# Kernel tuning notes

Measured on AMD Instinct MI355X. Metric: run time of the kernel, lower is better.

## Reference

```python
import jax, jax.numpy as jnp
import numpy as np

B, N, M, C = 2, 16384, 16, 64
D_HIDDEN = 64  # int(d * hidden_scale) with d=64, hidden_scale=1
BN_EPS = 1e-5


def setup_inputs() -> dict:
    key = jax.random.key(0)
    ks = jax.random.split(key, 10)
    s = 1.0 / np.sqrt(C)
    return {
        "center_feat": jax.random.normal(ks[0], (B, N, C), jnp.float32),
        "neighbor_feat": jax.random.normal(ks[1], (B, N, M, C), jnp.float32),
        "pos_enc": jax.random.normal(ks[2], (B, N, M, C), jnp.float32),
        "Wq": jax.random.normal(ks[3], (C, C), jnp.float32) * s,      # nn.Linear(d, d), no bias
        "Wkv": jax.random.normal(ks[4], (2 * C, C), jnp.float32) * s, # nn.Linear(d, 2d), no bias
        "W1": jax.random.normal(ks[5], (D_HIDDEN, C), jnp.float32) * s,  # 1x1 Conv2d(d, d_hidden)
        "bn_gamma": jnp.ones((D_HIDDEN,), jnp.float32),
        "bn_beta": jnp.zeros((D_HIDDEN,), jnp.float32),
        "bn_mean": jax.random.normal(ks[6], (D_HIDDEN,), jnp.float32) * 0.1,
        "bn_var": jax.random.uniform(ks[7], (D_HIDDEN,), jnp.float32, 0.5, 1.5),
        "W2": jax.random.normal(ks[8], (C, D_HIDDEN), jnp.float32) * (1.0 / np.sqrt(D_HIDDEN)),  # 1x1 Conv2d(d_hidden, d)
    }


def reference(center_feat, neighbor_feat, pos_enc, Wq, Wkv, W1, bn_gamma, bn_beta, bn_mean, bn_var, W2):
    # Q = Linear(center_feat): (B, N, C)
    Q = jnp.einsum("bnc,dc->bnd", center_feat, Wq)
    # K, V = chunk(Linear(neighbor_feat), 2): each (B, N, M, C)
    KV = jnp.einsum("bnmc,dc->bnmd", neighbor_feat, Wkv)
    K, V = jnp.split(KV, 2, axis=-1)
    # broadcast subtract + pos enc: (B, N, M, C)
    attn = Q[:, :, None, :] - K + pos_enc
    # mlp: 1x1 conv -> BN (eval, running stats) -> ReLU -> 1x1 conv (channel = last axis)
    h = jnp.einsum("bnmc,hc->bnmh", attn, W1)
    h = (h - bn_mean) * (bn_gamma / jnp.sqrt(bn_var + BN_EPS)) + bn_beta
    h = jax.nn.relu(h)
    attn = jnp.einsum("bnmh,ch->bnmc", h, W2)
    # softmax over neighbor dim M, weighted sum
    w = jax.nn.softmax(attn, axis=2)
    return jnp.sum(w * (V + pos_enc), axis=2)  # (B, N, C)
```

## Files before the change

kernel.cpp:

```cpp
#include <hip/hip_runtime.h>
#include <stdint.h>


#define NN 16384

typedef float f32x4 __attribute__((ext_vector_type(4)));
typedef short s16x8 __attribute__((ext_vector_type(8)));
typedef int   i32x4 __attribute__((ext_vector_type(4)));
typedef int   i32x2 __attribute__((ext_vector_type(2)));

__device__ __forceinline__ uint16_t f2bf(float f) {
  uint32_t u = __builtin_bit_cast(uint32_t, f);
  u += 0x7fffu + ((u >> 16) & 1u);
  return (uint16_t)(u >> 16);
}
__device__ __forceinline__ uint32_t pk2(float a, float b) {
  return (uint32_t)f2bf(a) | ((uint32_t)f2bf(b) << 16);
}

__device__ __forceinline__ f32x4 mma16(i32x4 a, i32x4 b, f32x4 c) {
  return __builtin_amdgcn_mfma_f32_16x16x32_bf16(
      __builtin_bit_cast(s16x8, a), __builtin_bit_cast(s16x8, b), c, 0, 0, 0);
}

__device__ __forceinline__ i32x4 afrag(const float* p) {
  f32x4 f0 = *(const f32x4*)p;
  f32x4 f1 = *(const f32x4*)(p + 16);
  i32x4 r;
  r.x = pk2(f0.x, f0.y); r.y = pk2(f0.z, f0.w);
  r.z = pk2(f1.x, f1.y); r.w = pk2(f1.z, f1.w);
  return r;
}

__device__ __forceinline__ void wstore(uint16_t* wp, int mat, int j, int k, float v) {
  int ct = j >> 4, jl = j & 15;
  int kt = k >> 5, r = k & 31;
  int kh = r >> 4, rr = r & 15;
  int gg = rr >> 2, e2 = rr & 3;
  int lanei = jl + (gg << 4);
  int e = kh * 4 + e2;
  wp[((mat * 8 + kt * 4 + ct) * 64 + lanei) * 8 + e] = f2bf(v);
}

__global__ void prep_weights(const float* __restrict__ Wq, const float* __restrict__ Wkv,
                             const float* __restrict__ W1, const float* __restrict__ gam,
                             const float* __restrict__ bet, const float* __restrict__ mu,
                             const float* __restrict__ var, const float* __restrict__ W2,
                             uint16_t* __restrict__ wp, float* __restrict__ b1) {
  int j = blockIdx.x * 16 + (threadIdx.x >> 4);
  int q = threadIdx.x & 15;
  float gp = gam[j] * rsqrtf(var[j] + 1e-5f);
  if (q == 0) b1[j] = bet[j] - gp * mu[j];
  for (int k = q * 4; k < q * 4 + 4; ++k) {
    float aq = 0.f, ak = 0.f;
    for (int c = 0; c < 64; ++c) {
      float w1 = W1[j * 64 + c];
      aq += w1 * Wq[c * 64 + k];
      ak += w1 * Wkv[c * 64 + k];
    }
    wstore(wp, 0, j, k, gp * aq);
    wstore(wp, 1, j, k, -gp * ak);
    wstore(wp, 2, j, k, gp * W1[j * 64 + k]);
    wstore(wp, 3, j, k, Wkv[(64 + j) * 64 + k]);
    wstore(wp, 4, j, k, W2[j * 64 + k]);
  }
}

#define W_LDS_ELEMS (5 * 4096)
#define HSTR 72

__device__ __forceinline__ i32x4 bfragld(const uint16_t* wlds, int mat, int kt, int ct, int lane) {
  return *(const i32x4*)(wlds + ((mat * 8 + kt * 4 + ct) * 64 + lane) * 8);
}

__global__ __launch_bounds__(256, 2) void vattn_main(
    const float* __restrict__ center, const float* __restrict__ nbr,
    const float* __restrict__ pos, const uint16_t* __restrict__ wp,
    const float* __restrict__ b1, float* __restrict__ out) {
  __shared__ uint16_t wlds[W_LDS_ELEMS];
  __shared__ uint16_t hlds[4 * 16 * HSTR];
  const int tid = threadIdx.x;
  {
    const i32x4* src = (const i32x4*)wp;
    i32x4* dst = (i32x4*)wlds;
#pragma unroll
    for (int i = 0; i < 10; ++i) dst[tid + 256 * i] = src[tid + 256 * i];
  }
  __syncthreads();

  const int w = tid >> 6;
  const int lane = tid & 63;
  const int l15 = lane & 15;
  const int g = lane >> 4;
  const int blk = blockIdx.x;
  const int b = blk >> 10;
  const int n0 = (blk & 1023) << 4;
  const long crow0 = (long)b * NN + n0;

  float b1v[4];
#pragma unroll
  for (int ct = 0; ct < 4; ++ct) b1v[ct] = b1[ct * 16 + l15];

  f32x4 qh[4];
#pragma unroll
  for (int ct = 0; ct < 4; ++ct) qh[ct] = (f32x4){0.f, 0.f, 0.f, 0.f};
  {
    const float* crow = center + (crow0 + l15) * 64 + g * 4;
    i32x4 ca0 = afrag(crow);
    i32x4 ca1 = afrag(crow + 32);
#pragma unroll
    for (int ct = 0; ct < 4; ++ct) {
      qh[ct] = mma16(ca0, bfragld(wlds, 0, 0, ct, lane), qh[ct]);
      qh[ct] = mma16(ca1, bfragld(wlds, 0, 1, ct, lane), qh[ct]);
      f32x4 bb = {b1v[ct], b1v[ct], b1v[ct], b1v[ct]};
      qh[ct] = qh[ct] + bb;
    }
  }

  uint16_t* hw = hlds + w * 16 * HSTR;

#pragma unroll
  for (int rt = 0; rt < 4; ++rt) {
    const int nl = (w << 2) + rt;
    const long nrow = crow0 + nl;
    const float* nrp = nbr + (nrow * 16 + l15) * 64 + g * 4;
    const float* prp = pos + (nrow * 16 + l15) * 64 + g * 4;
    i32x4 na0 = afrag(nrp), na1 = afrag(nrp + 32);
    i32x4 pa0 = afrag(prp), pa1 = afrag(prp + 32);

    float qb[4];
#pragma unroll
    for (int ct = 0; ct < 4; ++ct) qb[ct] = __shfl(qh[ct][rt], l15 + (w << 4), 64);

    f32x4 hb[4], vv[4];
#pragma unroll
    for (int ct = 0; ct < 4; ++ct) {
      hb[ct] = (f32x4){qb[ct], qb[ct], qb[ct], qb[ct]};
      vv[ct] = (f32x4){0.f, 0.f, 0.f, 0.f};
    }
#pragma unroll
    for (int ct = 0; ct < 4; ++ct) {
      hb[ct] = mma16(na0, bfragld(wlds, 1, 0, ct, lane), hb[ct]);
      hb[ct] = mma16(na1, bfragld(wlds, 1, 1, ct, lane), hb[ct]);
      hb[ct] = mma16(pa0, bfragld(wlds, 2, 0, ct, lane), hb[ct]);
      hb[ct] = mma16(pa1, bfragld(wlds, 2, 1, ct, lane), hb[ct]);
      vv[ct] = mma16(na0, bfragld(wlds, 3, 0, ct, lane), vv[ct]);
      vv[ct] = mma16(na1, bfragld(wlds, 3, 1, ct, lane), vv[ct]);
    }

#pragma unroll
    for (int ct = 0; ct < 4; ++ct)
#pragma unroll
      for (int r = 0; r < 4; ++r)
        hw[(4 * g + r) * HSTR + ct * 16 + l15] = f2bf(fmaxf(hb[ct][r], 0.f));
    asm volatile("s_waitcnt lgkmcnt(0)" ::: "memory");

    const uint16_t* hr = hw + l15 * HSTR + g * 4;
    i32x4 ha0, ha1;
    {
      i32x2 x = *(const i32x2*)(hr);
      i32x2 y = *(const i32x2*)(hr + 16);
      ha0.x = x.x; ha0.y = x.y; ha0.z = y.x; ha0.w = y.y;
    }
    {
      i32x2 x = *(const i32x2*)(hr + 32);
      i32x2 y = *(const i32x2*)(hr + 48);
      ha1.x = x.x; ha1.y = x.y; ha1.z = y.x; ha1.w = y.y;
    }
    f32x4 a2[4];
#pragma unroll
    for (int ct = 0; ct < 4; ++ct) {
      a2[ct] = (f32x4){0.f, 0.f, 0.f, 0.f};
      a2[ct] = mma16(ha0, bfragld(wlds, 4, 0, ct, lane), a2[ct]);
      a2[ct] = mma16(ha1, bfragld(wlds, 4, 1, ct, lane), a2[ct]);
    }

    const float* posrow = pos + nrow * 16 * 64;
    float ov[4];
#pragma unroll
    for (int ct = 0; ct < 4; ++ct) {
      f32x4 s = a2[ct];
      float mx = fmaxf(fmaxf(s.x, s.y), fmaxf(s.z, s.w));
      mx = fmaxf(mx, __shfl_xor(mx, 16, 64));
      mx = fmaxf(mx, __shfl_xor(mx, 32, 64));
      float e0 = __expf(s.x - mx), e1 = __expf(s.y - mx);
      float e2 = __expf(s.z - mx), e3 = __expf(s.w - mx);
      float sm = e0 + e1 + e2 + e3;
      sm += __shfl_xor(sm, 16, 64);
      sm += __shfl_xor(sm, 32, 64);
      const float* pp = posrow + (4 * g) * 64 + ct * 16 + l15;
      float ps = e0 * (vv[ct].x + pp[0])   + e1 * (vv[ct].y + pp[64]) +
                 e2 * (vv[ct].z + pp[128]) + e3 * (vv[ct].w + pp[192]);
      ps += __shfl_xor(ps, 16, 64);
      ps += __shfl_xor(ps, 32, 64);
      ov[ct] = ps / sm;
    }
    float val = (g == 0) ? ov[0] : (g == 1) ? ov[1] : (g == 2) ? ov[2] : ov[3];
    out[nrow * 64 + lane] = val;
  }
}

extern "C" void kernel_launch(void* const* d_in, const int* in_sizes, int n_in,
                              void* d_out, int out_size, void* d_ws, size_t ws_size,
                              hipStream_t stream) {
  const float* center = (const float*)d_in[0];
  const float* nbr    = (const float*)d_in[1];
  const float* pos    = (const float*)d_in[2];
  const float* Wq     = (const float*)d_in[3];
  const float* Wkv    = (const float*)d_in[4];
  const float* W1     = (const float*)d_in[5];
  const float* gam    = (const float*)d_in[6];
  const float* bet    = (const float*)d_in[7];
  const float* mu     = (const float*)d_in[8];
  const float* var    = (const float*)d_in[9];
  const float* W2     = (const float*)d_in[10];
  uint16_t* wp = (uint16_t*)d_ws;
  float* b1 = (float*)((char*)d_ws + 5 * 4096 * 2);
  prep_weights<<<4, 256, 0, stream>>>(Wq, Wkv, W1, gam, bet, mu, var, W2, wp, b1);
  vattn_main<<<2048, 256, 0, stream>>>(center, nbr, pos, wp, b1, (float*)d_out);
}
```

Baseline: 100.3 us.

## Compute transposed hidden layer in registers, drop LDS round-trip, prefetch next tile

The first MLP layer now uses weights as the A operand and activations as B, producing a transposed accumulator that maps directly onto the A-fragment layout of the second matmul. This removes the LDS staging buffer for the hidden activations and its wait. The Q projection is folded into the per-tile accumulation instead of being computed once and shuffled. Loads for the next neighbour/pos tile are double-buffered in registers, and occupancy is raised to 3 blocks per CU. In exchange the kernel uses more registers and does redundant Q matmuls per tile.

```diff
diff --git a/kernel.cpp b/kernel.cpp
--- a/kernel.cpp
+++ b/kernel.cpp
@@ -7,7 +7,6 @@
 typedef float f32x4 __attribute__((ext_vector_type(4)));
 typedef short s16x8 __attribute__((ext_vector_type(8)));
 typedef int   i32x4 __attribute__((ext_vector_type(4)));
-typedef int   i32x2 __attribute__((ext_vector_type(2)));
 
 __device__ __forceinline__ uint16_t f2bf(float f) {
   uint32_t u = __builtin_bit_cast(uint32_t, f);
@@ -23,13 +22,14 @@
       __builtin_bit_cast(s16x8, a), __builtin_bit_cast(s16x8, b), c, 0, 0, 0);
 }
 
-__device__ __forceinline__ i32x4 afrag(const float* p) {
-  f32x4 f0 = *(const f32x4*)p;
-  f32x4 f1 = *(const f32x4*)(p + 16);
+__device__ __forceinline__ i32x4 packfrag(f32x4 f0, f32x4 f1) {
   i32x4 r;
   r.x = pk2(f0.x, f0.y); r.y = pk2(f0.z, f0.w);
   r.z = pk2(f1.x, f1.y); r.w = pk2(f1.z, f1.w);
   return r;
+}
+__device__ __forceinline__ i32x4 afrag(const float* p) {
+  return packfrag(*(const f32x4*)p, *(const f32x4*)(p + 16));
 }
 
 __device__ __forceinline__ void wstore(uint16_t* wp, int mat, int j, int k, float v) {
@@ -67,18 +67,16 @@
 }
 
 #define W_LDS_ELEMS (5 * 4096)
-#define HSTR 72
 
 __device__ __forceinline__ i32x4 bfragld(const uint16_t* wlds, int mat, int kt, int ct, int lane) {
   return *(const i32x4*)(wlds + ((mat * 8 + kt * 4 + ct) * 64 + lane) * 8);
 }
 
-__global__ __launch_bounds__(256, 2) void vattn_main(
+__global__ __launch_bounds__(256, 3) void vattn_main(
     const float* __restrict__ center, const float* __restrict__ nbr,
     const float* __restrict__ pos, const uint16_t* __restrict__ wp,
     const float* __restrict__ b1, float* __restrict__ out) {
   __shared__ uint16_t wlds[W_LDS_ELEMS];
-  __shared__ uint16_t hlds[4 * 16 * HSTR];
   const int tid = threadIdx.x;
   {
     const i32x4* src = (const i32x4*)wp;
@@ -95,78 +93,72 @@
   const int blk = blockIdx.x;
   const int b = blk >> 10;
   const int n0 = (blk & 1023) << 4;
-  const long crow0 = (long)b * NN + n0;
-
-  float b1v[4];
-#pragma unroll
-  for (int ct = 0; ct < 4; ++ct) b1v[ct] = b1[ct * 16 + l15];
-
-  f32x4 qh[4];
-#pragma unroll
-  for (int ct = 0; ct < 4; ++ct) qh[ct] = (f32x4){0.f, 0.f, 0.f, 0.f};
-  {
-    const float* crow = center + (crow0 + l15) * 64 + g * 4;
-    i32x4 ca0 = afrag(crow);
-    i32x4 ca1 = afrag(crow + 32);
-#pragma unroll
-    for (int ct = 0; ct < 4; ++ct) {
-      qh[ct] = mma16(ca0, bfragld(wlds, 0, 0, ct, lane), qh[ct]);
-      qh[ct] = mma16(ca1, bfragld(wlds, 0, 1, ct, lane), qh[ct]);
-      f32x4 bb = {b1v[ct], b1v[ct], b1v[ct], b1v[ct]};
-      qh[ct] = qh[ct] + bb;
-    }
-  }
-
-  uint16_t* hw = hlds + w * 16 * HSTR;
+  const long nbase = (long)b * NN + n0 + (w << 2);
+
+  f32x4 binit[4];
+#pragma unroll
+  for (int ct = 0; ct < 4; ++ct)
+#pragma unroll
+    for (int r = 0; r < 4; ++r) binit[ct][r] = b1[ct * 16 + 4 * g + r];
+
+  f32x4 raw[2][8];
+#define ISSUE(BUF, RT) do {                                                   \
+    const float* nrp_ = nbr + (((nbase + (RT)) * 16 + l15) * 64) + g * 4;     \
+    const float* prp_ = pos + (((nbase + (RT)) * 16 + l15) * 64) + g * 4;     \
+    raw[BUF][0] = *(const f32x4*)nrp_;        raw[BUF][1] = *(const f32x4*)(nrp_ + 16); \
+    raw[BUF][2] = *(const f32x4*)(nrp_ + 32); raw[BUF][3] = *(const f32x4*)(nrp_ + 48); \
+    raw[BUF][4] = *(const f32x4*)prp_;        raw[BUF][5] = *(const f32x4*)(prp_ + 16); \
+    raw[BUF][6] = *(const f32x4*)(prp_ + 32); raw[BUF][7] = *(const f32x4*)(prp_ + 48); \
+  } while (0)
+
+  ISSUE(0, 0);
 
 #pragma unroll
   for (int rt = 0; rt < 4; ++rt) {
-    const int nl = (w << 2) + rt;
-    const long nrow = crow0 + nl;
-    const float* nrp = nbr + (nrow * 16 + l15) * 64 + g * 4;
-    const float* prp = pos + (nrow * 16 + l15) * 64 + g * 4;
-    i32x4 na0 = afrag(nrp), na1 = afrag(nrp + 32);
-    i32x4 pa0 = afrag(prp), pa1 = afrag(prp + 32);
-
-    float qb[4];
-#pragma unroll
-    for (int ct = 0; ct < 4; ++ct) qb[ct] = __shfl(qh[ct][rt], l15 + (w << 4), 64);
-
-    f32x4 hb[4], vv[4];
-#pragma unroll
-    for (int ct = 0; ct < 4; ++ct) {
-      hb[ct] = (f32x4){qb[ct], qb[ct], qb[ct], qb[ct]};
+    if (rt < 3) ISSUE((rt + 1) & 1, rt + 1);
+    const int buf = rt & 1;
+    const long nrow = nbase + rt;
+
+    const float* crp = center + nrow * 64 + g * 4;
+    i32x4 ca0 = afrag(crp), ca1 = afrag(crp + 32);
+
+    i32x4 na0 = packfrag(raw[buf][0], raw[buf][1]);
+    i32x4 na1 = packfrag(raw[buf][2], raw[buf][3]);
+    i32x4 pa0 = packfrag(raw[buf][4], raw[buf][5]);
+    i32x4 pa1 = packfrag(raw[buf][6], raw[buf][7]);
+
+    f32x4 h[4];
+#pragma unroll
+    for (int ct = 0; ct < 4; ++ct) {
+      h[ct] = binit[ct];
+      h[ct] = mma16(bfragld(wlds, 0, 0, ct, lane), ca0, h[ct]);
+      h[ct] = mma16(bfragld(wlds, 0, 1, ct, lane), ca1, h[ct]);
+      h[ct] = mma16(bfragld(wlds, 1, 0, ct, lane), na0, h[ct]);
+      h[ct] = mma16(bfragld(wlds, 1, 1, ct, lane), na1, h[ct]);
+      h[ct] = mma16(bfragld(wlds, 2, 0, ct, lane), pa0, h[ct]);
+      h[ct] = mma16(bfragld(wlds, 2, 1, ct, lane), pa1, h[ct]);
+    }
+
+    f32x4 vv[4];
+#pragma unroll
+    for (int ct = 0; ct < 4; ++ct) {
       vv[ct] = (f32x4){0.f, 0.f, 0.f, 0.f};
-    }
-#pragma unroll
-    for (int ct = 0; ct < 4; ++ct) {
-      hb[ct] = mma16(na0, bfragld(wlds, 1, 0, ct, lane), hb[ct]);
-      hb[ct] = mma16(na1, bfragld(wlds, 1, 1, ct, lane), hb[ct]);
-      hb[ct] = mma16(pa0, bfragld(wlds, 2, 0, ct, lane), hb[ct]);
-      hb[ct] = mma16(pa1, bfragld(wlds, 2, 1, ct, lane), hb[ct]);
       vv[ct] = mma16(na0, bfragld(wlds, 3, 0, ct, lane), vv[ct]);
       vv[ct] = mma16(na1, bfragld(wlds, 3, 1, ct, lane), vv[ct]);
     }
 
-#pragma unroll
-    for (int ct = 0; ct < 4; ++ct)
-#pragma unroll
-      for (int r = 0; r < 4; ++r)
-        hw[(4 * g + r) * HSTR + ct * 16 + l15] = f2bf(fmaxf(hb[ct][r], 0.f));
-    asm volatile("s_waitcnt lgkmcnt(0)" ::: "memory");
-
-    const uint16_t* hr = hw + l15 * HSTR + g * 4;
     i32x4 ha0, ha1;
     {
-      i32x2 x = *(const i32x2*)(hr);
-      i32x2 y = *(const i32x2*)(hr + 16);
-      ha0.x = x.x; ha0.y = x.y; ha0.z = y.x; ha0.w = y.y;
-    }
-    {
-      i32x2 x = *(const i32x2*)(hr + 32);
-      i32x2 y = *(const i32x2*)(hr + 48);
-      ha1.x = x.x; ha1.y = x.y; ha1.z = y.x; ha1.w = y.y;
-    }
+      f32x4 r0, r1, r2, r3;
+#pragma unroll
+      for (int r = 0; r < 4; ++r) {
+        r0[r] = fmaxf(h[0][r], 0.f); r1[r] = fmaxf(h[1][r], 0.f);
+        r2[r] = fmaxf(h[2][r], 0.f); r3[r] = fmaxf(h[3][r], 0.f);
+      }
+      ha0 = packfrag(r0, r1);
+      ha1 = packfrag(r2, r3);
+    }
+
     f32x4 a2[4];
 #pragma unroll
     for (int ct = 0; ct < 4; ++ct) {
@@ -198,6 +190,7 @@
     float val = (g == 0) ? ov[0] : (g == 1) ? ov[1] : (g == 2) ? ov[2] : ov[3];
     out[nrow * 64 + lane] = val;
   }
+#undef ISSUE
 }
 
 extern "C" void kernel_launch(void* const* d_in, const int* in_sizes, int n_in,
```

Result: faster. 95.66 us (-4.7%).
